# Kernel optimization log

Hardware: AMD Instinct MI355X
Metric: run time of the kernel (lower is better)

Reference implementation:

```python
import jax, jax.numpy as jnp
import numpy as np

B, C_IN, IMG = 16, 3, 224
P = 8                      # patch size (kernel == stride)
D = 256                    # d_model == embed_dim
NH = 8                     # num heads
HD = D // NH               # head dim = 32
G = IMG // P               # 28x28 patch grid
N = G * G                  # 784 patches
MRD = 31                   # max_relative_dist
T = 2 * MRD - 1            # 61
SCALE = HD ** -0.5


def setup_inputs() -> dict:
    key = jax.random.key(0)
    ks = jax.random.split(key, 11)
    std = 0.02
    yy, xx = jnp.meshgrid(jnp.arange(G), jnp.arange(G), indexing='ij')
    pos = jnp.stack([yy.ravel(), xx.ravel()], axis=-1).astype(jnp.int32)  # (N,2)
    return {
        'cur_frame': jax.random.normal(ks[0], (B, C_IN, IMG, IMG), jnp.float32),
        'prev_frame': jax.random.normal(ks[1], (B, C_IN, IMG, IMG), jnp.float32),
        'conv_w': jax.random.normal(ks[2], (D, C_IN, P, P), jnp.float32) * std,
        'conv_b': jnp.zeros((D,), jnp.float32),
        'q_w': jax.random.normal(ks[3], (D, D), jnp.float32) * std,
        'q_b': jnp.zeros((D,), jnp.float32),
        'kv_w': jax.random.normal(ks[4], (2 * D, D), jnp.float32) * std,
        'kv_b': jnp.zeros((2 * D,), jnp.float32),
        'proj_w': jax.random.normal(ks[5], (D, D), jnp.float32) * std,
        'proj_b': jnp.zeros((D,), jnp.float32),
        'bias_table': jax.random.normal(ks[6], (T * T, NH), jnp.float32) * std,
        'cur_pos': pos,
        'prev_pos': pos,
    }


def _patch_embed(x, w, b):
    # Conv2d with kernel==stride==P (non-overlapping patches)
    y = jax.lax.conv_general_dilated(
        x, w, window_strides=(P, P), padding='VALID',
        dimension_numbers=('NCHW', 'OIHW', 'NCHW'))
    y = y + b[None, :, None, None]
    Bb, Dd, h, wd = y.shape
    return y.reshape(Bb, Dd, h * wd).transpose(0, 2, 1)  # (B, N, D)


def reference(cur_frame, prev_frame, conv_w, conv_b, q_w, q_b, kv_w, kv_b,
              proj_w, proj_b, bias_table, cur_pos, prev_pos):
    cur = _patch_embed(cur_frame, conv_w, conv_b)    # (B, N, D)
    prev = _patch_embed(prev_frame, conv_w, conv_b)  # (B, N, D)

    q = (cur @ q_w.T + q_b).reshape(B, N, NH, HD).transpose(0, 2, 1, 3) * SCALE
    kv = prev @ kv_w.T + kv_b                        # (B, N, 2D)
    k = kv[..., :D].reshape(B, N, NH, HD).transpose(0, 2, 1, 3)
    v = kv[..., D:].reshape(B, N, NH, HD).transpose(0, 2, 1, 3)

    attn = jnp.einsum('bhqd,bhkd->bhqk', q, k)       # (B, NH, N, N)

    # relative position bias gather: idx = (dy+30)*61 + (dx+30)
    rel = cur_pos[:, None, :] - prev_pos[None, :, :]             # (N, N, 2)
    idx = (rel[..., 0] + (MRD - 1)) * T + (rel[..., 1] + (MRD - 1))
    bias = bias_table[idx].transpose(2, 0, 1)                    # (NH, N, N)

    attn = jax.nn.softmax(attn + bias[None], axis=-1)
    x = jnp.einsum('bhqk,bhkd->bqhd', attn, v).reshape(B, N, D)
    return x @ proj_w.T + proj_b
```

## Files before the change

kernel.cpp:

```cpp
#include <hip/hip_runtime.h>

#define B_ 16
#define NP 784
#define D_ 256
#define NH_ 8
#define HD_ 32
#define KEMB 192
#define SCALE_ 0.17677669529663687f
#define LOG2E_ 1.4426950408889634f

typedef __attribute__((ext_vector_type(4))) float f32x4;
typedef __attribute__((ext_vector_type(8))) short bf16x8;
typedef __attribute__((ext_vector_type(4))) short bf16x4;

__device__ __forceinline__ unsigned short f2bf(float f) {
    union { float f; unsigned int u; } v; v.f = f;
    unsigned int u = v.u;
    unsigned int r = (u + 0x7fffu + ((u >> 16) & 1u)) >> 16;
    return (unsigned short)r;
}

__device__ __forceinline__ unsigned int cvtpk(float a, float b) {
    unsigned int r;
    asm("v_cvt_pk_bf16_f32 %0, %1, %2" : "=v"(r) : "v"(a), "v"(b));
    return r;
}

__device__ __forceinline__ float fexp2(float x) {
#if __has_builtin(__builtin_amdgcn_exp2f)
    return __builtin_amdgcn_exp2f(x);
#else
    return exp2f(x);
#endif
}

__device__ __forceinline__ void gl_lds16(const unsigned short* g, unsigned short* l) {
    __builtin_amdgcn_global_load_lds(
        (const __attribute__((address_space(1))) unsigned int*)(const void*)g,
        (__attribute__((address_space(3))) unsigned int*)(void*)l, 16, 0, 0);
}

__global__ __launch_bounds__(256) void conv_prep(
    const float* __restrict__ cur, const float* __restrict__ prev,
    const float* __restrict__ conv_w32, const float* __restrict__ bias,
    const float* __restrict__ q_w32, const float* __restrict__ kv_w32,
    const float* __restrict__ pr_w32,
    unsigned short* __restrict__ w_q, unsigned short* __restrict__ w_kv,
    unsigned short* __restrict__ w_pr,
    const float* __restrict__ bt, float* __restrict__ bto,
    unsigned short* __restrict__ outp)
{
    const int tid = threadIdx.x;
    if (blockIdx.x >= 784) {
        int bi = blockIdx.x - 784;
        if (bi < 256) {
            int i = (bi * 256 + tid) * 4;
            const float* s; unsigned short* dp; int off;
            if (i < 65536)       { s = q_w32;  dp = w_q;  off = i; }
            else if (i < 196608) { s = kv_w32; dp = w_kv; off = i - 65536; }
            else                 { s = pr_w32; dp = w_pr; off = i - 196608; }
            float4 v = *(const float4*)(s + off);
            dp[off + 0] = f2bf(v.x); dp[off + 1] = f2bf(v.y);
            dp[off + 2] = f2bf(v.z); dp[off + 3] = f2bf(v.w);
        } else {
            int i = (bi - 256) * 256 + tid;
            if (i < 29768) {
                int h = i / 3721, idx = i - h * 3721;
                bto[i] = bt[idx * NH_ + h] * LOG2E_;
            }
        }
        return;
    }
    __shared__ __align__(16) unsigned short At[32 * 64];
    __shared__ __align__(16) unsigned short Bt[256 * 64];
    const int lane = tid & 63, wid = tid >> 6;
    const int lo = lane & 15, hi = lane >> 4;
    const int m0 = blockIdx.x * 32;
    const float* asrc;
    unsigned short* adst;
    {
        int row = tid >> 3, seg = tid & 7;
        int m = m0 + row;
        int fb = m / NP, n = m - fb * NP;
        int py = n / 28, px = n - py * 28;
        const float* F = (fb >= 16 ? prev + (size_t)(fb - 16) * 150528 : cur + (size_t)fb * 150528);
        asrc = F + (py * 8 + seg) * 224 + px * 8;
        adst = At + row * 64 + ((seg ^ (row & 7)) * 8);
    }
    f32x4 acc[2][4] = {};
#pragma unroll
    for (int kt = 0; kt < 3; ++kt) {
        __syncthreads();
#pragma unroll
        for (int i = 0; i < 8; ++i) {
            int s = i * 256 + tid;
            int row = s >> 3, j = s & 7, seg = j ^ (row & 7);
            const float* wsrc = conv_w32 + row * KEMB + kt * 64 + seg * 8;
            float4 b0 = *(const float4*)(wsrc);
            float4 b1 = *(const float4*)(wsrc + 4);
            union { unsigned int u[4]; bf16x8 v; } bv;
            bv.u[0] = cvtpk(b0.x, b0.y); bv.u[1] = cvtpk(b0.z, b0.w);
            bv.u[2] = cvtpk(b1.x, b1.y); bv.u[3] = cvtpk(b1.z, b1.w);
            *(bf16x8*)(void*)(Bt + row * 64 + j * 8) = bv.v;
        }
        {
            const float* src = asrc + kt * 50176;
            float4 a0 = *(const float4*)(src);
            float4 a1 = *(const float4*)(src + 4);
            union { unsigned int u[4]; bf16x8 v; } ov;
            ov.u[0] = cvtpk(a0.x, a0.y); ov.u[1] = cvtpk(a0.z, a0.w);
            ov.u[2] = cvtpk(a1.x, a1.y); ov.u[3] = cvtpk(a1.z, a1.w);
            *(bf16x8*)(void*)(adst) = ov.v;
        }
        __syncthreads();
#pragma unroll
        for (int kk = 0; kk < 2; ++kk) {
            bf16x8 af[2], bfv[4];
#pragma unroll
            for (int f = 0; f < 2; ++f) {
                int rowa = f * 16 + lo;
                af[f] = *(const bf16x8*)(const void*)(At + rowa * 64 + (((kk * 4 + hi) ^ (rowa & 7)) * 8));
            }
#pragma unroll
            for (int f = 0; f < 4; ++f) {
                int rowb = wid * 64 + f * 16 + lo;
                bfv[f] = *(const bf16x8*)(const void*)(Bt + rowb * 64 + (((kk * 4 + hi) ^ (rowb & 7)) * 8));
            }
#pragma unroll
            for (int fr = 0; fr < 2; ++fr)
#pragma unroll
                for (int fc = 0; fc < 4; ++fc)
                    acc[fr][fc] = __builtin_amdgcn_mfma_f32_16x16x32_bf16(af[fr], bfv[fc], acc[fr][fc], 0, 0, 0);
        }
    }
#pragma unroll
    for (int fr = 0; fr < 2; ++fr)
#pragma unroll
        for (int fc = 0; fc < 4; ++fc)
#pragma unroll
            for (int r = 0; r < 4; ++r) {
                int m = m0 + fr * 16 + hi * 4 + r;
                int c = wid * 64 + fc * 16 + lo;
                outp[(size_t)m * D_ + c] = f2bf(acc[fr][fc][r] + bias[c]);
            }
}

__global__ __launch_bounds__(256) void gemm_qkv(
    const unsigned short* __restrict__ emb,
    const unsigned short* __restrict__ w_q, const float* __restrict__ q_b,
    const unsigned short* __restrict__ w_kv, const float* __restrict__ kv_b,
    unsigned short* __restrict__ q_h, unsigned short* __restrict__ k_h,
    unsigned short* __restrict__ v_t)
{
    __shared__ __align__(16) unsigned short At[128 * 64];
    __shared__ __align__(16) unsigned short Bt[128 * 64];
    const int tid = threadIdx.x;
    const int lo = tid & 15, hi = (tid >> 4) & 3, wid = tid >> 6;
    const int m0 = blockIdx.x * 128;
    const int y = blockIdx.y;
    const bool iskv = y >= 2;
    const unsigned short* Abase = iskv ? emb + (size_t)12544 * D_ : emb;
    const unsigned short* W = iskv ? w_kv : w_q;
    const float* bias = iskv ? kv_b : q_b;
    const int n0 = (iskv ? y - 2 : y) * 128;
    const int wr = wid >> 1, wc = wid & 1;
    const int wvb = wid * 512;
    f32x4 acc[4][4] = {};
#pragma unroll
    for (int kt = 0; kt < 4; ++kt) {
        const int k0 = kt * 64;
        __syncthreads();
#pragma unroll
        for (int i = 0; i < 4; ++i) {
            int s = i * 256 + tid;
            int row = s >> 3, seg = (s & 7) ^ (row & 7);
            gl_lds16(Abase + (size_t)(m0 + row) * D_ + k0 + seg * 8, At + i * 2048 + wvb);
            gl_lds16(W + (size_t)(n0 + row) * D_ + k0 + seg * 8, Bt + i * 2048 + wvb);
        }
        __syncthreads();
#pragma unroll
        for (int kk = 0; kk < 2; ++kk) {
            bf16x8 af[4], bfv[4];
#pragma unroll
            for (int f = 0; f < 4; ++f) {
                int rowa = wr * 64 + f * 16 + lo;
                af[f] = *(const bf16x8*)(const void*)(At + rowa * 64 + (((kk * 4 + hi) ^ (rowa & 7)) * 8));
                int rowb = wc * 64 + f * 16 + lo;
                bfv[f] = *(const bf16x8*)(const void*)(Bt + rowb * 64 + (((kk * 4 + hi) ^ (rowb & 7)) * 8));
            }
#pragma unroll
            for (int fr = 0; fr < 4; ++fr)
#pragma unroll
                for (int fc = 0; fc < 4; ++fc)
                    acc[fr][fc] = __builtin_amdgcn_mfma_f32_16x16x32_bf16(af[fr], bfv[fc], acc[fr][fc], 0, 0, 0);
        }
    }
#pragma unroll
    for (int fr = 0; fr < 4; ++fr)
#pragma unroll
        for (int fc = 0; fc < 4; ++fc)
#pragma unroll
            for (int r = 0; r < 4; ++r) {
                int m = m0 + wr * 64 + fr * 16 + hi * 4 + r;
                int c = n0 + wc * 64 + fc * 16 + lo;
                float val = acc[fr][fc][r] + bias[c];
                int b = m / NP, n = m - (m / NP) * NP;
                if (!iskv) {
                    int h = c >> 5, d = c & 31;
                    q_h[(((size_t)(b * NH_ + h)) * NP + n) * HD_ + d] = f2bf(val * (SCALE_ * LOG2E_));
                } else if (c < D_) {
                    int h = c >> 5, d = c & 31;
                    k_h[(((size_t)(b * NH_ + h)) * NP + n) * HD_ + d] = f2bf(val);
                } else {
                    int cc = c - D_; int h = cc >> 5, d = cc & 31;
                    v_t[(((size_t)(b * NH_ + h)) * HD_ + d) * NP + n] = f2bf(val);
                }
            }
}

__global__ __launch_bounds__(256) void gemm_px(
    const unsigned short* __restrict__ A, const unsigned short* __restrict__ W,
    const float* __restrict__ bias, float* __restrict__ outp)
{
    __shared__ __align__(16) unsigned short At[32 * 64];
    __shared__ __align__(16) unsigned short Bt[128 * 64];
    const int tid = threadIdx.x;
    const int lo = tid & 15, hi = (tid >> 4) & 3, wid = tid >> 6;
    const int m0 = blockIdx.x * 32, n0 = blockIdx.y * 128;
    const int wr = wid >> 1, wc = wid & 1;
    const int wvb = wid * 512;
    f32x4 acc[4] = {};
#pragma unroll
    for (int kt = 0; kt < 4; ++kt) {
        const int k0 = kt * 64;
        __syncthreads();
        {
            int row = tid >> 3, seg = (tid & 7) ^ ((tid >> 3) & 7);
            gl_lds16(A + (size_t)(m0 + row) * D_ + k0 + seg * 8, At + wvb);
        }
#pragma unroll
        for (int i = 0; i < 4; ++i) {
            int s = i * 256 + tid;
            int row = s >> 3, seg = (s & 7) ^ (row & 7);
            gl_lds16(W + (size_t)(n0 + row) * D_ + k0 + seg * 8, Bt + i * 2048 + wvb);
        }
        __syncthreads();
#pragma unroll
        for (int kk = 0; kk < 2; ++kk) {
            bf16x8 af, bfv[4];
            {
                int rowa = wr * 16 + lo;
                af = *(const bf16x8*)(const void*)(At + rowa * 64 + (((kk * 4 + hi) ^ (rowa & 7)) * 8));
            }
#pragma unroll
            for (int f = 0; f < 4; ++f) {
                int rowb = wc * 64 + f * 16 + lo;
                bfv[f] = *(const bf16x8*)(const void*)(Bt + rowb * 64 + (((kk * 4 + hi) ^ (rowb & 7)) * 8));
            }
#pragma unroll
            for (int fc = 0; fc < 4; ++fc)
                acc[fc] = __builtin_amdgcn_mfma_f32_16x16x32_bf16(af, bfv[fc], acc[fc], 0, 0, 0);
        }
    }
#pragma unroll
    for (int fc = 0; fc < 4; ++fc)
#pragma unroll
        for (int r = 0; r < 4; ++r) {
            int m = m0 + wr * 16 + hi * 4 + r;
            int c = n0 + wc * 64 + fc * 16 + lo;
            outp[(size_t)m * D_ + c] = acc[fc][r] + bias[c];
        }
}

__global__ __launch_bounds__(448) void attn_k(
    const unsigned short* __restrict__ qh, const unsigned short* __restrict__ kh,
    const unsigned short* __restrict__ vt, const float* __restrict__ bias_t,
    const int* __restrict__ cpos, const int* __restrict__ ppos,
    unsigned short* __restrict__ x)
{
    __shared__ __align__(16) unsigned short Vt[2][32 * 64];
    __shared__ __align__(16) float2 Bp[1890];
    __shared__ int ktab[196];
    const int tid = threadIdx.x;
    const int lane = tid & 63, wid = tid >> 6;
    const int lo = lane & 15, hi = lane >> 4;
    const int bid = blockIdx.x;
    const int h = bid & 7;
    const int t2 = bid >> 3;
    const int b = t2 / 7;
    const int qt = t2 - b * 7;
    const int bh = b * 8 + h;
    const int q0 = qt * 112 + wid * 16;
    const int blbase = (qt * 4 + 3) * 61;

    {
        const float* bsl = bias_t + h * 3721 + blbase;
        for (int i = tid; i < 1890; i += 448)
            Bp[i] = float2{ bsl[i], bsl[i + 1] };
        if (tid < 196) {
            int kc = tid * 4;
            ktab[tid] = ppos[2 * kc] * 61 + ppos[2 * kc + 1];
        }
    }

    bf16x8 qf;
    int qb;
    {
        int qr = q0 + lo;
        qf = *(const bf16x8*)(const void*)(qh + (((size_t)bh * NP) + qr) * HD_ + hi * 8);
        qb = cpos[qr * 2] * 61 + cpos[qr * 2 + 1] + 1860 - blbase;
    }

    const unsigned short* kbase = kh + (size_t)bh * NP * HD_;
    const unsigned short* vbase = vt + (size_t)bh * HD_ * NP;
    const int tv = tid - 192, sd = tv >> 3, ssg = tv & 7;
    bf16x8 vst = {};

    auto issue = [&](int kt) {
        if (tid >= 192)
            vst = *(const bf16x8*)(const void*)(vbase + sd * NP + kt * 64 + ssg * 8);
    };
    auto stage = [&](int buf) {
        if (tid >= 192) {
            int f = ssg >> 2;
            int j4 = ((ssg >> 1) & 1) * 4;
            int blkA = f * 4 + ((2 * ssg) & 3);
            int blkB = f * 4 + ((2 * ssg + 1) & 3);
            bf16x4 vlo = { vst[0], vst[1], vst[2], vst[3] };
            bf16x4 vhi = { vst[4], vst[5], vst[6], vst[7] };
            *(bf16x4*)(void*)(Vt[buf] + sd * 64 + ((blkA ^ (sd & 7)) * 8) + j4) = vlo;
            *(bf16x4*)(void*)(Vt[buf] + sd * 64 + ((blkB ^ (sd & 7)) * 8) + j4) = vhi;
        }
    };

    f32x4 o[2] = {};
    float lr = 0.f;

    issue(0);
    stage(0);
    for (int kt = 0; kt < 13; ++kt) {
        int cur = kt & 1;
        int k0 = kt * 64;
        if (kt < 12) issue(kt + 1);
        bf16x8 kf[4];
#pragma unroll
        for (int g = 0; g < 4; ++g)
            kf[g] = *(const bf16x8*)(const void*)(kbase + (size_t)(k0 + g * 16 + lo) * HD_ + hi * 8);
        __syncthreads();
        bool tail = (kt == 12);

        f32x4 bc[4];
#pragma unroll
        for (int g = 0; g < 4; ++g) {
            if (tail && g > 0) {
                bc[g] = f32x4{ -1e30f, -1e30f, -1e30f, -1e30f };
            } else {
                int kbg = ktab[kt * 16 + g * 4 + hi];
                int off = qb - kbg - 3;
                float2 pA = Bp[off];
                float2 pB = Bp[off + 2];
                bc[g][0] = pB.y; bc[g][1] = pB.x; bc[g][2] = pA.y; bc[g][3] = pA.x;
            }
        }
        f32x4 s[4];
#pragma unroll
        for (int g = 0; g < 4; ++g)
            s[g] = __builtin_amdgcn_mfma_f32_16x16x32_bf16(kf[g], qf, bc[g], 0, 0, 0);
        unsigned int c[4][2];
        float psum = 0.f;
#pragma unroll
        for (int g = 0; g < 4; ++g) {
            float p0 = fexp2(s[g][0]);
            float p1 = fexp2(s[g][1]);
            float p2 = fexp2(s[g][2]);
            float p3 = fexp2(s[g][3]);
            psum += (p0 + p1) + (p2 + p3);
            c[g][0] = cvtpk(p0, p1);
            c[g][1] = cvtpk(p2, p3);
        }
        lr += psum;
#pragma unroll
        for (int f = 0; f < 2; ++f) {
            union { unsigned int u[4]; bf16x8 v; } pu;
            pu.u[0] = c[2 * f][0]; pu.u[1] = c[2 * f][1];
            pu.u[2] = c[2 * f + 1][0]; pu.u[3] = c[2 * f + 1][1];
#pragma unroll
            for (int cc = 0; cc < 2; ++cc) {
                int d = cc * 16 + lo;
                bf16x8 vf = *(const bf16x8*)(const void*)(Vt[cur] + d * 64 + (((f * 4 + hi) ^ (d & 7)) * 8));
                o[cc] = __builtin_amdgcn_mfma_f32_16x16x32_bf16(pu.v, vf, o[cc], 0, 0, 0);
            }
        }
        if (kt < 12) stage(cur ^ 1);
    }
    lr += __shfl_xor(lr, 16);
    lr += __shfl_xor(lr, 32);
    float li = 1.0f / lr;
    float lro[4];
#pragma unroll
    for (int r = 0; r < 4; ++r)
        lro[r] = __shfl(li, (lane & 48) | (hi * 4 + r));
#pragma unroll
    for (int cc = 0; cc < 2; ++cc)
#pragma unroll
        for (int r = 0; r < 4; ++r) {
            int qr = q0 + hi * 4 + r;
            float val = o[cc][r] * lro[r];
            x[((size_t)b * NP + qr) * D_ + h * HD_ + cc * 16 + lo] = f2bf(val);
        }
}

extern "C" void kernel_launch(void* const* d_in, const int* in_sizes, int n_in,
                              void* d_out, int out_size, void* d_ws, size_t ws_size,
                              hipStream_t stream)
{
    const float* cur    = (const float*)d_in[0];
    const float* prev   = (const float*)d_in[1];
    const float* conv_w = (const float*)d_in[2];
    const float* conv_b = (const float*)d_in[3];
    const float* q_w    = (const float*)d_in[4];
    const float* q_b    = (const float*)d_in[5];
    const float* kv_w   = (const float*)d_in[6];
    const float* kv_b   = (const float*)d_in[7];
    const float* proj_w = (const float*)d_in[8];
    const float* proj_b = (const float*)d_in[9];
    const float* btab   = (const float*)d_in[10];
    const int* cpos     = (const int*)d_in[11];
    const int* ppos     = (const int*)d_in[12];

    char* ws = (char*)d_ws;
    unsigned short* w_q    = (unsigned short*)(ws + 98304);
    unsigned short* w_kv   = (unsigned short*)(ws + 229376);
    unsigned short* w_pr   = (unsigned short*)(ws + 491520);
    float* bias_t          = (float*)(ws + 622592);
    unsigned short* emb    = (unsigned short*)(ws + 10256384);
    unsigned short* q_h    = (unsigned short*)(ws + 23101440);
    unsigned short* k_h    = (unsigned short*)(ws + 29523968);
    unsigned short* v_t    = (unsigned short*)(ws + 35946496);
    unsigned short* xb     = (unsigned short*)(ws + 42369024);

    conv_prep<<<1157, 256, 0, stream>>>(cur, prev, conv_w, conv_b,
                                        q_w, kv_w, proj_w, w_q, w_kv, w_pr,
                                        btab, bias_t, emb);
    gemm_qkv<<<dim3(98, 6), 256, 0, stream>>>(emb, w_q, q_b, w_kv, kv_b, q_h, k_h, v_t);
    attn_k<<<896, 448, 0, stream>>>(q_h, k_h, v_t, bias_t, cpos, ppos, xb);
    gemm_px<<<dim3(392, 2), 256, 0, stream>>>(xb, w_pr, proj_b, (float*)d_out);

    (void)in_sizes; (void)n_in; (void)out_size; (void)ws_size;
}
```

Baseline: 77.46 us.

## Pre-permute V in QKV GEMM epilogue and read V fragments directly from global

The QKV GEMM epilogue now writes V in a padded, pre-permuted per-64-key tile layout that matches the MFMA operand order. The attention kernel then loads V fragments straight from global/L2 instead of double-buffering them through LDS. This drops the staging threads, the LDS writes and the per-iteration barrier. The tail tile skips the fully masked half. The attention output buffer also reuses the embedding workspace. The risk is that each wave now issues redundant global V loads, since all 7 waves read the same V tile, and these global loads have more latency than LDS.

```diff
diff --git a/kernel.cpp b/kernel.cpp
--- a/kernel.cpp
+++ b/kernel.cpp
@@ -6,6 +6,7 @@
 #define NH_ 8
 #define HD_ 32
 #define KEMB 192
+#define VPITCH 832
 #define SCALE_ 0.17677669529663687f
 #define LOG2E_ 1.4426950408889634f
 
@@ -213,7 +214,11 @@
                     k_h[(((size_t)(b * NH_ + h)) * NP + n) * HD_ + d] = f2bf(val);
                 } else {
                     int cc = c - D_; int h = cc >> 5, d = cc & 31;
-                    v_t[(((size_t)(b * NH_ + h)) * HD_ + d) * NP + n] = f2bf(val);
+                    int tile = n >> 6, kk2 = n & 63;
+                    int ssg = kk2 >> 3, jj = kk2 & 7, half = jj >> 2;
+                    int col = ((ssg >> 2) * 4 + ((2 * ssg + half) & 3)) * 8
+                            + ((ssg >> 1) & 1) * 4 + (jj & 3);
+                    v_t[(((size_t)(b * NH_ + h)) * HD_ + d) * VPITCH + tile * 64 + col] = f2bf(val);
                 }
             }
 }
@@ -278,7 +283,6 @@
     const int* __restrict__ cpos, const int* __restrict__ ppos,
     unsigned short* __restrict__ x)
 {
-    __shared__ __align__(16) unsigned short Vt[2][32 * 64];
     __shared__ __align__(16) float2 Bp[1890];
     __shared__ int ktab[196];
     const int tid = threadIdx.x;
@@ -310,44 +314,21 @@
         qf = *(const bf16x8*)(const void*)(qh + (((size_t)bh * NP) + qr) * HD_ + hi * 8);
         qb = cpos[qr * 2] * 61 + cpos[qr * 2 + 1] + 1860 - blbase;
     }
+    __syncthreads();
 
     const unsigned short* kbase = kh + (size_t)bh * NP * HD_;
-    const unsigned short* vbase = vt + (size_t)bh * HD_ * NP;
-    const int tv = tid - 192, sd = tv >> 3, ssg = tv & 7;
-    bf16x8 vst = {};
-
-    auto issue = [&](int kt) {
-        if (tid >= 192)
-            vst = *(const bf16x8*)(const void*)(vbase + sd * NP + kt * 64 + ssg * 8);
-    };
-    auto stage = [&](int buf) {
-        if (tid >= 192) {
-            int f = ssg >> 2;
-            int j4 = ((ssg >> 1) & 1) * 4;
-            int blkA = f * 4 + ((2 * ssg) & 3);
-            int blkB = f * 4 + ((2 * ssg + 1) & 3);
-            bf16x4 vlo = { vst[0], vst[1], vst[2], vst[3] };
-            bf16x4 vhi = { vst[4], vst[5], vst[6], vst[7] };
-            *(bf16x4*)(void*)(Vt[buf] + sd * 64 + ((blkA ^ (sd & 7)) * 8) + j4) = vlo;
-            *(bf16x4*)(void*)(Vt[buf] + sd * 64 + ((blkB ^ (sd & 7)) * 8) + j4) = vhi;
-        }
-    };
+    const unsigned short* vbase = vt + (size_t)bh * HD_ * VPITCH;
 
     f32x4 o[2] = {};
     float lr = 0.f;
 
-    issue(0);
-    stage(0);
     for (int kt = 0; kt < 13; ++kt) {
-        int cur = kt & 1;
         int k0 = kt * 64;
-        if (kt < 12) issue(kt + 1);
+        bool tail = (kt == 12);
         bf16x8 kf[4];
 #pragma unroll
         for (int g = 0; g < 4; ++g)
             kf[g] = *(const bf16x8*)(const void*)(kbase + (size_t)(k0 + g * 16 + lo) * HD_ + hi * 8);
-        __syncthreads();
-        bool tail = (kt == 12);
 
         f32x4 bc[4];
 #pragma unroll
@@ -381,17 +362,24 @@
         lr += psum;
 #pragma unroll
         for (int f = 0; f < 2; ++f) {
+            if (tail && f == 1) break;
             union { unsigned int u[4]; bf16x8 v; } pu;
             pu.u[0] = c[2 * f][0]; pu.u[1] = c[2 * f][1];
             pu.u[2] = c[2 * f + 1][0]; pu.u[3] = c[2 * f + 1][1];
 #pragma unroll
             for (int cc = 0; cc < 2; ++cc) {
                 int d = cc * 16 + lo;
-                bf16x8 vf = *(const bf16x8*)(const void*)(Vt[cur] + d * 64 + (((f * 4 + hi) ^ (d & 7)) * 8));
+                const unsigned short* vsrc = vbase + (size_t)d * VPITCH + k0 + (f * 4 + hi) * 8;
+                bf16x8 vf;
+                if (!tail) {
+                    vf = *(const bf16x8*)(const void*)vsrc;
+                } else {
+                    bf16x4 v4 = *(const bf16x4*)(const void*)vsrc;
+                    vf = bf16x8{ v4[0], v4[1], v4[2], v4[3], 0, 0, 0, 0 };
+                }
                 o[cc] = __builtin_amdgcn_mfma_f32_16x16x32_bf16(pu.v, vf, o[cc], 0, 0, 0);
             }
         }
-        if (kt < 12) stage(cur ^ 1);
     }
     lr += __shfl_xor(lr, 16);
     lr += __shfl_xor(lr, 32);
@@ -434,10 +422,10 @@
     unsigned short* w_pr   = (unsigned short*)(ws + 491520);
     float* bias_t          = (float*)(ws + 622592);
     unsigned short* emb    = (unsigned short*)(ws + 10256384);
+    unsigned short* xb     = emb;
     unsigned short* q_h    = (unsigned short*)(ws + 23101440);
     unsigned short* k_h    = (unsigned short*)(ws + 29523968);
     unsigned short* v_t    = (unsigned short*)(ws + 35946496);
-    unsigned short* xb     = (unsigned short*)(ws + 42369024);
 
     conv_prep<<<1157, 256, 0, stream>>>(cur, prev, conv_w, conv_b,
                                         q_w, kv_w, proj_w, w_q, w_kv, w_pr,
```

After: 124.5 us. 1.61x slower.

## Preload entire V tile into LDS and drop per-iteration barriers

Applied to the files above, without the earlier changes.

The attention kernel used to stream V through a double-buffered 64-key LDS tile, with a __syncthreads every key iteration and only some waves doing the staging. It now has all threads load the whole swizzled 32x832 V slice for the block into LDS once, with one barrier before the main loop. This removes 13 block-wide barriers and the staging work inside the loop. In exchange, LDS per block grows from roughly 8KB to 53KB for V, which can reduce how many blocks fit on a CU. It also adds an exposed load phase up front with nothing to overlap it.

```diff
diff --git a/kernel.cpp b/kernel.cpp
--- a/kernel.cpp
+++ b/kernel.cpp
@@ -278,7 +278,7 @@
     const int* __restrict__ cpos, const int* __restrict__ ppos,
     unsigned short* __restrict__ x)
 {
-    __shared__ __align__(16) unsigned short Vt[2][32 * 64];
+    __shared__ __align__(16) unsigned short Vt[32 * 832];
     __shared__ __align__(16) float2 Bp[1890];
     __shared__ int ktab[196];
     const int tid = threadIdx.x;
@@ -311,43 +311,37 @@
         qb = cpos[qr * 2] * 61 + cpos[qr * 2 + 1] + 1860 - blbase;
     }
 
-    const unsigned short* kbase = kh + (size_t)bh * NP * HD_;
-    const unsigned short* vbase = vt + (size_t)bh * HD_ * NP;
-    const int tv = tid - 192, sd = tv >> 3, ssg = tv & 7;
-    bf16x8 vst = {};
-
-    auto issue = [&](int kt) {
-        if (tid >= 192)
-            vst = *(const bf16x8*)(const void*)(vbase + sd * NP + kt * 64 + ssg * 8);
-    };
-    auto stage = [&](int buf) {
-        if (tid >= 192) {
+    {
+        const unsigned short* vbase = vt + (size_t)bh * HD_ * NP;
+        for (int t = tid; t < 3328; t += 448) {
+            int kt = t >> 8, s = t & 255;
+            int sd = s >> 3, ssg = s & 7;
+            bf16x8 vv = *(const bf16x8*)(const void*)(vbase + sd * NP + kt * 64 + ssg * 8);
             int f = ssg >> 2;
             int j4 = ((ssg >> 1) & 1) * 4;
             int blkA = f * 4 + ((2 * ssg) & 3);
             int blkB = f * 4 + ((2 * ssg + 1) & 3);
-            bf16x4 vlo = { vst[0], vst[1], vst[2], vst[3] };
-            bf16x4 vhi = { vst[4], vst[5], vst[6], vst[7] };
-            *(bf16x4*)(void*)(Vt[buf] + sd * 64 + ((blkA ^ (sd & 7)) * 8) + j4) = vlo;
-            *(bf16x4*)(void*)(Vt[buf] + sd * 64 + ((blkB ^ (sd & 7)) * 8) + j4) = vhi;
-        }
-    };
+            bf16x4 vlo = { vv[0], vv[1], vv[2], vv[3] };
+            bf16x4 vhi = { vv[4], vv[5], vv[6], vv[7] };
+            unsigned short* row = Vt + sd * 832 + kt * 64;
+            *(bf16x4*)(void*)(row + ((blkA ^ (sd & 7)) * 8) + j4) = vlo;
+            *(bf16x4*)(void*)(row + ((blkB ^ (sd & 7)) * 8) + j4) = vhi;
+        }
+    }
+    __syncthreads();
+
+    const unsigned short* kbase = kh + (size_t)bh * NP * HD_;
 
     f32x4 o[2] = {};
     float lr = 0.f;
 
-    issue(0);
-    stage(0);
     for (int kt = 0; kt < 13; ++kt) {
-        int cur = kt & 1;
         int k0 = kt * 64;
-        if (kt < 12) issue(kt + 1);
+        bool tail = (kt == 12);
         bf16x8 kf[4];
 #pragma unroll
         for (int g = 0; g < 4; ++g)
             kf[g] = *(const bf16x8*)(const void*)(kbase + (size_t)(k0 + g * 16 + lo) * HD_ + hi * 8);
-        __syncthreads();
-        bool tail = (kt == 12);
 
         f32x4 bc[4];
 #pragma unroll
@@ -387,11 +381,10 @@
 #pragma unroll
             for (int cc = 0; cc < 2; ++cc) {
                 int d = cc * 16 + lo;
-                bf16x8 vf = *(const bf16x8*)(const void*)(Vt[cur] + d * 64 + (((f * 4 + hi) ^ (d & 7)) * 8));
+                bf16x8 vf = *(const bf16x8*)(const void*)(Vt + d * 832 + k0 + (((f * 4 + hi) ^ (d & 7)) * 8));
                 o[cc] = __builtin_amdgcn_mfma_f32_16x16x32_bf16(pu.v, vf, o[cc], 0, 0, 0);
             }
         }
-        if (kt < 12) stage(cur ^ 1);
     }
     lr += __shfl_xor(lr, 16);
     lr += __shfl_xor(lr, 32);
```

After: 80.08 us. 3.4% more time.

## Process two query sub-tiles per wave to reuse K/V tiles in attention

Applied to the files above, without the earlier changes.

Each attention wave now computes 32 query rows instead of 16, reusing the loaded K fragments and staged V tile for two score/PV passes. Blocks cover 224 queries, the grid shrinks to 512 blocks, and the relative-bias shared slice is enlarged to cover 8 grid rows. This cuts K/V global loads and LDS staging per query, at the cost of more registers, fewer blocks, and some wasted work on clamped rows in the last tile.

```diff
diff --git a/kernel.cpp b/kernel.cpp
--- a/kernel.cpp
+++ b/kernel.cpp
@@ -279,7 +279,7 @@
     unsigned short* __restrict__ x)
 {
     __shared__ __align__(16) unsigned short Vt[2][32 * 64];
-    __shared__ __align__(16) float2 Bp[1890];
+    __shared__ __align__(16) float2 Bp[2136];
     __shared__ int ktab[196];
     const int tid = threadIdx.x;
     const int lane = tid & 63, wid = tid >> 6;
@@ -287,15 +287,15 @@
     const int bid = blockIdx.x;
     const int h = bid & 7;
     const int t2 = bid >> 3;
-    const int b = t2 / 7;
-    const int qt = t2 - b * 7;
+    const int b = t2 >> 2;
+    const int qt = t2 & 3;
     const int bh = b * 8 + h;
-    const int q0 = qt * 112 + wid * 16;
-    const int blbase = (qt * 4 + 3) * 61;
+    const int q0 = qt * 224 + wid * 32;
+    const int blbase = (qt * 8 + 3) * 61;
 
     {
         const float* bsl = bias_t + h * 3721 + blbase;
-        for (int i = tid; i < 1890; i += 448)
+        for (int i = tid; i < 2134; i += 448)
             Bp[i] = float2{ bsl[i], bsl[i + 1] };
         if (tid < 196) {
             int kc = tid * 4;
@@ -303,12 +303,15 @@
         }
     }
 
-    bf16x8 qf;
-    int qb;
+    bf16x8 qf0, qf1;
+    int qb0, qb1;
     {
-        int qr = q0 + lo;
-        qf = *(const bf16x8*)(const void*)(qh + (((size_t)bh * NP) + qr) * HD_ + hi * 8);
-        qb = cpos[qr * 2] * 61 + cpos[qr * 2 + 1] + 1860 - blbase;
+        int qr0 = q0 + lo;       if (qr0 > 783) qr0 = 783;
+        int qr1 = q0 + 16 + lo;  if (qr1 > 783) qr1 = 783;
+        qf0 = *(const bf16x8*)(const void*)(qh + (((size_t)bh * NP) + qr0) * HD_ + hi * 8);
+        qf1 = *(const bf16x8*)(const void*)(qh + (((size_t)bh * NP) + qr1) * HD_ + hi * 8);
+        qb0 = cpos[qr0 * 2] * 61 + cpos[qr0 * 2 + 1] + 1860 - blbase;
+        qb1 = cpos[qr1 * 2] * 61 + cpos[qr1 * 2 + 1] + 1860 - blbase;
     }
 
     const unsigned short* kbase = kh + (size_t)bh * NP * HD_;
@@ -333,8 +336,8 @@
         }
     };
 
-    f32x4 o[2] = {};
-    float lr = 0.f;
+    f32x4 o0[2] = {}, o1[2] = {};
+    float lr0 = 0.f, lr1 = 0.f;
 
     issue(0);
     stage(0);
@@ -349,64 +352,117 @@
         __syncthreads();
         bool tail = (kt == 12);
 
-        f32x4 bc[4];
-#pragma unroll
-        for (int g = 0; g < 4; ++g) {
-            if (tail && g > 0) {
-                bc[g] = f32x4{ -1e30f, -1e30f, -1e30f, -1e30f };
-            } else {
-                int kbg = ktab[kt * 16 + g * 4 + hi];
-                int off = qb - kbg - 3;
-                float2 pA = Bp[off];
-                float2 pB = Bp[off + 2];
-                bc[g][0] = pB.y; bc[g][1] = pB.x; bc[g][2] = pA.y; bc[g][3] = pA.x;
-            }
-        }
-        f32x4 s[4];
-#pragma unroll
-        for (int g = 0; g < 4; ++g)
-            s[g] = __builtin_amdgcn_mfma_f32_16x16x32_bf16(kf[g], qf, bc[g], 0, 0, 0);
-        unsigned int c[4][2];
-        float psum = 0.f;
-#pragma unroll
-        for (int g = 0; g < 4; ++g) {
-            float p0 = fexp2(s[g][0]);
-            float p1 = fexp2(s[g][1]);
-            float p2 = fexp2(s[g][2]);
-            float p3 = fexp2(s[g][3]);
-            psum += (p0 + p1) + (p2 + p3);
-            c[g][0] = cvtpk(p0, p1);
-            c[g][1] = cvtpk(p2, p3);
-        }
-        lr += psum;
-#pragma unroll
-        for (int f = 0; f < 2; ++f) {
-            union { unsigned int u[4]; bf16x8 v; } pu;
-            pu.u[0] = c[2 * f][0]; pu.u[1] = c[2 * f][1];
-            pu.u[2] = c[2 * f + 1][0]; pu.u[3] = c[2 * f + 1][1];
-#pragma unroll
-            for (int cc = 0; cc < 2; ++cc) {
-                int d = cc * 16 + lo;
-                bf16x8 vf = *(const bf16x8*)(const void*)(Vt[cur] + d * 64 + (((f * 4 + hi) ^ (d & 7)) * 8));
-                o[cc] = __builtin_amdgcn_mfma_f32_16x16x32_bf16(pu.v, vf, o[cc], 0, 0, 0);
+        {
+            f32x4 bc[4];
+#pragma unroll
+            for (int g = 0; g < 4; ++g) {
+                if (tail && g > 0) {
+                    bc[g] = f32x4{ -1e30f, -1e30f, -1e30f, -1e30f };
+                } else {
+                    int kbg = ktab[kt * 16 + g * 4 + hi];
+                    int off = qb0 - kbg - 3;
+                    float2 pA = Bp[off];
+                    float2 pB = Bp[off + 2];
+                    bc[g][0] = pB.y; bc[g][1] = pB.x; bc[g][2] = pA.y; bc[g][3] = pA.x;
+                }
+            }
+            f32x4 s[4];
+#pragma unroll
+            for (int g = 0; g < 4; ++g)
+                s[g] = __builtin_amdgcn_mfma_f32_16x16x32_bf16(kf[g], qf0, bc[g], 0, 0, 0);
+            unsigned int c[4][2];
+            float psum = 0.f;
+#pragma unroll
+            for (int g = 0; g < 4; ++g) {
+                float p0 = fexp2(s[g][0]);
+                float p1 = fexp2(s[g][1]);
+                float p2 = fexp2(s[g][2]);
+                float p3 = fexp2(s[g][3]);
+                psum += (p0 + p1) + (p2 + p3);
+                c[g][0] = cvtpk(p0, p1);
+                c[g][1] = cvtpk(p2, p3);
+            }
+            lr0 += psum;
+#pragma unroll
+            for (int f = 0; f < 2; ++f) {
+                union { unsigned int u[4]; bf16x8 v; } pu;
+                pu.u[0] = c[2 * f][0]; pu.u[1] = c[2 * f][1];
+                pu.u[2] = c[2 * f + 1][0]; pu.u[3] = c[2 * f + 1][1];
+#pragma unroll
+                for (int cc = 0; cc < 2; ++cc) {
+                    int d = cc * 16 + lo;
+                    bf16x8 vf = *(const bf16x8*)(const void*)(Vt[cur] + d * 64 + (((f * 4 + hi) ^ (d & 7)) * 8));
+                    o0[cc] = __builtin_amdgcn_mfma_f32_16x16x32_bf16(pu.v, vf, o0[cc], 0, 0, 0);
+                }
+            }
+        }
+        {
+            f32x4 bc[4];
+#pragma unroll
+            for (int g = 0; g < 4; ++g) {
+                if (tail && g > 0) {
+                    bc[g] = f32x4{ -1e30f, -1e30f, -1e30f, -1e30f };
+                } else {
+                    int kbg = ktab[kt * 16 + g * 4 + hi];
+                    int off = qb1 - kbg - 3;
+                    float2 pA = Bp[off];
+                    float2 pB = Bp[off + 2];
+                    bc[g][0] = pB.y; bc[g][1] = pB.x; bc[g][2] = pA.y; bc[g][3] = pA.x;
+                }
+            }
+            f32x4 s[4];
+#pragma unroll
+            for (int g = 0; g < 4; ++g)
+                s[g] = __builtin_amdgcn_mfma_f32_16x16x32_bf16(kf[g], qf1, bc[g], 0, 0, 0);
+            unsigned int c[4][2];
+            float psum = 0.f;
+#pragma unroll
+            for (int g = 0; g < 4; ++g) {
+                float p0 = fexp2(s[g][0]);
+                float p1 = fexp2(s[g][1]);
+                float p2 = fexp2(s[g][2]);
+                float p3 = fexp2(s[g][3]);
+                psum += (p0 + p1) + (p2 + p3);
+                c[g][0] = cvtpk(p0, p1);
+                c[g][1] = cvtpk(p2, p3);
+            }
+            lr1 += psum;
+#pragma unroll
+            for (int f = 0; f < 2; ++f) {
+                union { unsigned int u[4]; bf16x8 v; } pu;
+                pu.u[0] = c[2 * f][0]; pu.u[1] = c[2 * f][1];
+                pu.u[2] = c[2 * f + 1][0]; pu.u[3] = c[2 * f + 1][1];
+#pragma unroll
+                for (int cc = 0; cc < 2; ++cc) {
+                    int d = cc * 16 + lo;
+                    bf16x8 vf = *(const bf16x8*)(const void*)(Vt[cur] + d * 64 + (((f * 4 + hi) ^ (d & 7)) * 8));
+                    o1[cc] = __builtin_amdgcn_mfma_f32_16x16x32_bf16(pu.v, vf, o1[cc], 0, 0, 0);
+                }
             }
         }
         if (kt < 12) stage(cur ^ 1);
     }
-    lr += __shfl_xor(lr, 16);
-    lr += __shfl_xor(lr, 32);
-    float li = 1.0f / lr;
-    float lro[4];
-#pragma unroll
-    for (int r = 0; r < 4; ++r)
-        lro[r] = __shfl(li, (lane & 48) | (hi * 4 + r));
+    lr0 += __shfl_xor(lr0, 16);
+    lr0 += __shfl_xor(lr0, 32);
+    lr1 += __shfl_xor(lr1, 16);
+    lr1 += __shfl_xor(lr1, 32);
+    float li0 = 1.0f / lr0, li1 = 1.0f / lr1;
+    float lro0[4], lro1[4];
+#pragma unroll
+    for (int r = 0; r < 4; ++r) {
+        lro0[r] = __shfl(li0, (lane & 48) | (hi * 4 + r));
+        lro1[r] = __shfl(li1, (lane & 48) | (hi * 4 + r));
+    }
 #pragma unroll
     for (int cc = 0; cc < 2; ++cc)
 #pragma unroll
         for (int r = 0; r < 4; ++r) {
             int qr = q0 + hi * 4 + r;
-            float val = o[cc][r] * lro[r];
-            x[((size_t)b * NP + qr) * D_ + h * HD_ + cc * 16 + lo] = f2bf(val);
+            if (qr < NP)
+                x[((size_t)b * NP + qr) * D_ + h * HD_ + cc * 16 + lo] = f2bf(o0[cc][r] * lro0[r]);
+            int qs = q0 + 16 + hi * 4 + r;
+            if (qs < NP)
+                x[((size_t)b * NP + qs) * D_ + h * HD_ + cc * 16 + lo] = f2bf(o1[cc][r] * lro1[r]);
         }
 }
 
@@ -443,7 +499,7 @@
                                         q_w, kv_w, proj_w, w_q, w_kv, w_pr,
                                         btab, bias_t, emb);
     gemm_qkv<<<dim3(98, 6), 256, 0, stream>>>(emb, w_q, q_b, w_kv, kv_b, q_h, k_h, v_t);
-    attn_k<<<896, 448, 0, stream>>>(q_h, k_h, v_t, bias_t, cpos, ppos, xb);
+    attn_k<<<512, 448, 0, stream>>>(q_h, k_h, v_t, bias_t, cpos, ppos, xb);
     gemm_px<<<dim3(392, 2), 256, 0, stream>>>(xb, w_pr, proj_b, (float*)d_out);
 
     (void)in_sizes; (void)n_in; (void)out_size; (void)ws_size;
```

After: 73.80 us, median of 2. 4.7% less time.
